# Performance work log

Measured on AMD Instinct MI355X. Metric: run time of the kernel, lower is better.

Reference implementation:

```python
import jax, jax.numpy as jnp
from jax import lax
import numpy as np

B, N, NP, NS = 32, 4096, 512, 16
C = 256            # seed_feat_dim
RADIUS = 0.3
EPS = 1e-5         # BatchNorm eps
HID = 128


def setup_inputs() -> dict:
    key = jax.random.key(0)
    ks = jax.random.split(key, 8)
    xyz = jax.random.normal(ks[0], (B, N, 3), jnp.float32)
    features = jax.random.normal(ks[1], (B, C, N), jnp.float32)
    seed_xyz = jax.random.normal(ks[2], (B, N, 3), jnp.float32)
    c_in = C + 3  # use_xyz=True -> mlp[0] += 3
    def conv_w(k, cin, cout):
        return jax.random.normal(k, (cout, cin), jnp.float32) * (1.0 / np.sqrt(cin))
    w1 = conv_w(ks[3], c_in, HID)
    w2 = conv_w(ks[4], HID, HID)
    w3 = conv_w(ks[5], HID, HID)
    ones = jnp.ones((HID,), jnp.float32)
    zeros = jnp.zeros((HID,), jnp.float32)
    return dict(xyz=xyz, features=features, seed_xyz=seed_xyz,
                w1=w1, g1=ones, be1=zeros,
                w2=w2, g2=ones, be2=zeros,
                w3=w3, g3=ones, be3=zeros)


def furthest_point_sample(pts, npoint):
    # pts: (B, N, 3) -> (B, npoint) int32
    Bb, Nn, _ = pts.shape
    first = jnp.zeros((Bb,), jnp.int32)
    dists0 = jnp.full((Bb, Nn), 1e10, pts.dtype)
    def step(carry, _):
        dists, last = carry
        lp = jnp.take_along_axis(pts, last[:, None, None], axis=1)  # (B,1,3)
        d = jnp.sum((pts - lp) ** 2, axis=-1)                        # (B,N)
        dists = jnp.minimum(dists, d)
        nxt = jnp.argmax(dists, axis=-1).astype(jnp.int32)
        return (dists, nxt), nxt
    _, rest = lax.scan(step, (dists0, first), None, length=npoint - 1)
    return jnp.concatenate([first[None, :], rest], axis=0).T  # (B, npoint)


def ball_query(new_xyz, xyz, radius, nsample):
    # new_xyz: (B,NP,3), xyz: (B,N,3) -> (B,NP,nsample) int32
    d2 = jnp.sum((new_xyz[:, :, None, :] - xyz[:, None, :, :]) ** 2, axis=-1)  # (B,NP,N)
    Nn = xyz.shape[1]
    # first `nsample` indices (in index order) inside radius, like the CUDA kernel
    score = jnp.where(d2 < radius * radius, jnp.arange(Nn, dtype=jnp.int32)[None, None, :], Nn)
    neg_vals, _ = lax.top_k(-score, nsample)   # largest of -score = smallest indices
    idx = -neg_vals                            # (B,NP,nsample)
    valid = idx < Nn
    idx = jnp.where(valid, idx, idx[:, :, 0:1])  # pad with first hit (query point itself)
    return idx


def _conv_bn_relu(x, w, g, be):
    # x: (B,Cin,NP,NS); 1x1 Conv2d (no bias, bn=True) + BatchNorm2d (training stats) + ReLU
    y = jnp.einsum('oc,bcps->bops', w, x)
    m = y.mean(axis=(0, 2, 3))
    v = y.var(axis=(0, 2, 3))
    y = (y - m[None, :, None, None]) * (g / jnp.sqrt(v + EPS))[None, :, None, None] + be[None, :, None, None]
    return jax.nn.relu(y)


def reference(xyz, features, seed_xyz, w1, g1, be1, w2, g2, be2, w3, g3, be3):
    # sampling == 'seed_fps'
    sample_inds = furthest_point_sample(seed_xyz, NP)                 # (B,NP)
    new_xyz = jnp.take_along_axis(xyz, sample_inds[:, :, None], axis=1)  # (B,NP,3)
    idx = ball_query(new_xyz, xyz, RADIUS, NS)                        # (B,NP,NS)
    grouped_xyz = jax.vmap(lambda p, i: p[i])(xyz, idx)               # (B,NP,NS,3)
    grouped_xyz = (grouped_xyz - new_xyz[:, :, None, :]) / RADIUS     # normalize_xyz=True
    grouped_feat = jax.vmap(lambda f, i: f[:, i])(features, idx)      # (B,C,NP,NS)
    x = jnp.concatenate([grouped_xyz.transpose(0, 3, 1, 2), grouped_feat], axis=1)  # (B,3+C,NP,NS)
    x = _conv_bn_relu(x, w1, g1, be1)
    x = _conv_bn_relu(x, w2, g2, be2)
    x = _conv_bn_relu(x, w3, g3, be3)
    new_features = jnp.max(x, axis=-1)                                # (B,128,NP)
    return new_xyz, new_features, sample_inds
```

## Files before the change

### kernel.cpp

```cpp
#include <hip/hip_runtime.h>
#include <cstdint>
#include <cstddef>

#define B   32
#define N   4096
#define NP  512
#define NS  16
#define C   256
#define CIN 259
#define HID 128
#define SB  (NP*NS)
#define S   (B*SB)
#define EPSF 1e-5f

#define FPS_BLOCKS 32
#define TR_BLOCKS  (B*256)
#define PREP_BLOCKS 64

typedef __attribute__((ext_vector_type(8))) short short8;
typedef __attribute__((ext_vector_type(4))) float floatx4;

__device__ __forceinline__ float bf2f(unsigned short u) {
    return __uint_as_float(((unsigned)u) << 16);
}
__device__ __forceinline__ unsigned short f2bf(float f) {
    unsigned u = __float_as_uint(f);
    return (unsigned short)((u + 0x7FFFu + ((u >> 16) & 1u)) >> 16);
}

__device__ __forceinline__ int wave_max_i32(int x) {
    int y;
    y = __builtin_amdgcn_update_dpp(0, x, 0x111, 0xf, 0xf, true); x = (y > x) ? y : x;
    y = __builtin_amdgcn_update_dpp(0, x, 0x112, 0xf, 0xf, true); x = (y > x) ? y : x;
    y = __builtin_amdgcn_update_dpp(0, x, 0x114, 0xf, 0xf, true); x = (y > x) ? y : x;
    y = __builtin_amdgcn_update_dpp(0, x, 0x118, 0xf, 0xf, true); x = (y > x) ? y : x;
    y = __builtin_amdgcn_update_dpp(0, x, 0x142, 0xa, 0xf, true); x = (y > x) ? y : x;
    y = __builtin_amdgcn_update_dpp(0, x, 0x143, 0xc, 0xf, true); x = (y > x) ? y : x;
    return __builtin_amdgcn_readlane(x, 63);
}
__device__ __forceinline__ unsigned wave_max_u32(unsigned x) {
    unsigned y;
    y = (unsigned)__builtin_amdgcn_update_dpp(0, (int)x, 0x111, 0xf, 0xf, true); x = (y > x) ? y : x;
    y = (unsigned)__builtin_amdgcn_update_dpp(0, (int)x, 0x112, 0xf, 0xf, true); x = (y > x) ? y : x;
    y = (unsigned)__builtin_amdgcn_update_dpp(0, (int)x, 0x114, 0xf, 0xf, true); x = (y > x) ? y : x;
    y = (unsigned)__builtin_amdgcn_update_dpp(0, (int)x, 0x118, 0xf, 0xf, true); x = (y > x) ? y : x;
    y = (unsigned)__builtin_amdgcn_update_dpp(0, (int)x, 0x142, 0xa, 0xf, true); x = (y > x) ? y : x;
    y = (unsigned)__builtin_amdgcn_update_dpp(0, (int)x, 0x143, 0xc, 0xf, true); x = (y > x) ? y : x;
    return (unsigned)__builtin_amdgcn_readlane((int)x, 63);
}

__device__ __forceinline__ unsigned long long umax64(unsigned long long a, unsigned long long b) {
    return (b > a) ? b : a;
}

__global__ __launch_bounds__(512) void fused_front_kernel(
        const float* __restrict__ seed, const float* __restrict__ xyz,
        const float* __restrict__ feat, const float* __restrict__ w1,
        const float* __restrict__ w2, const float* __restrict__ w3,
        unsigned short* __restrict__ featT, unsigned short* __restrict__ w1fb,
        unsigned short* __restrict__ w2b, unsigned short* __restrict__ w3b,
        float* __restrict__ stats, int* __restrict__ inds,
        float* __restrict__ out_newxyz, float* __restrict__ out_inds_f) {
    __shared__ float smem[3 * N];
    __shared__ __align__(16) unsigned long long skey[2][8];
    __shared__ __align__(16) float4 scoord[2][8];
    __shared__ int lhist[NP];
    int bid = blockIdx.x;
    int t = threadIdx.x;

    if (bid >= FPS_BLOCKS) {
        int hb = bid - FPS_BLOCKS;
        if (hb < TR_BLOCKS) {
            float* ls = smem;
            int b2 = hb >> 8, rem = hb & 255;
            int ct = rem >> 5, jt = rem & 31;
            int c0 = ct * 32, j0 = jt * 128;
            const float* src = feat + (size_t)b2 * C * N;
            #pragma unroll
            for (int i = 0; i < 8; i++) {
                int lin = t + 512 * i;
                int jj = lin & 127, cc = lin >> 7;
                ls[cc * 129 + jj] = src[(size_t)(c0 + cc) * N + j0 + jj];
            }
            __syncthreads();
            int c8 = t & 3, jj = t >> 2;
            unsigned pk[4];
            #pragma unroll
            for (int q = 0; q < 4; q++) {
                float f0 = ls[(c8 * 8 + 2 * q) * 129 + jj];
                float f1 = ls[(c8 * 8 + 2 * q + 1) * 129 + jj];
                pk[q] = (unsigned)f2bf(f0) | ((unsigned)f2bf(f1) << 16);
            }
            *(uint4*)&featT[((size_t)b2 * N + j0 + jj) * 256 + c0 + c8 * 8] =
                make_uint4(pk[0], pk[1], pk[2], pk[3]);
        } else {
            int i0 = (hb - TR_BLOCKS) * 512 + t;
            if (i0 < 256 * HID) { int o = i0 >> 8, k = i0 & 255; w1fb[i0] = f2bf(w1[o * CIN + 3 + k]); }
            if (i0 < HID * HID) { w2b[i0] = f2bf(w2[i0]); w3b[i0] = f2bf(w3[i0]); }
            if (i0 < 3 * 512) stats[i0] = 0.f;
        }
        return;
    }

    int b = bid;
    const float* sp = seed + (size_t)b * N * 3;
    float px[8], py[8], pz[8], dloc[8];
    #pragma unroll
    for (int u = 0; u < 8; u++) {
        int i = t + 512 * u;
        px[u] = sp[i * 3 + 0]; py[u] = sp[i * 3 + 1]; pz[u] = sp[i * 3 + 2];
        dloc[u] = 1e10f;
    }
    if (t == 0) lhist[0] = 0;
    float lx = sp[0], ly = sp[1], lz = sp[2];
    int lane = t & 63, w = t >> 6;
    for (int k = 1; k < NP; k++) {
        float bv = -1.f; int bi = 0;
        float bx = 0.f, by = 0.f, bz = 0.f;
        #pragma unroll
        for (int u = 0; u < 8; u++) {
            int i = t + 512 * u;
            float dx = __fsub_rn(px[u], lx);
            float dy = __fsub_rn(py[u], ly);
            float dz = __fsub_rn(pz[u], lz);
            float d  = __fadd_rn(__fadd_rn(__fmul_rn(dx, dx), __fmul_rn(dy, dy)), __fmul_rn(dz, dz));
            float dm = fminf(dloc[u], d);
            dloc[u] = dm;
            bool bt = dm > bv;
            bv = bt ? dm : bv;
            bi = bt ? i : bi;
            bx = bt ? px[u] : bx;
            by = bt ? py[u] : by;
            bz = bt ? pz[u] : bz;
        }
        int wm = wave_max_i32(__float_as_int(bv));
        unsigned cand = (__float_as_int(bv) == wm) ? ~(unsigned)bi : 0u;
        unsigned winv = wave_max_u32(cand);
        int wbi = (int)(~winv);
        int par = k & 1;
        if (lane == (wbi & 63)) {
            skey[par][w] = (((unsigned long long)(unsigned)wm) << 12) | (unsigned)(4095 - wbi);
            scoord[par][w] = make_float4(bx, by, bz, 0.f);
        }
        __syncthreads();
        const ulonglong2* kp = (const ulonglong2*)&skey[par][0];
        ulonglong2 q0 = kp[0], q1 = kp[1], q2 = kp[2], q3 = kp[3];
        unsigned long long a = umax64(q0.x, q0.y);
        unsigned long long c2 = umax64(q1.x, q1.y);
        unsigned long long e = umax64(q2.x, q2.y);
        unsigned long long g = umax64(q3.x, q3.y);
        unsigned long long h = umax64(umax64(a, c2), umax64(e, g));
        int gi = 4095 - (int)(h & 0xFFFull);
        int ws = (gi & 511) >> 6;
        float4 wc = scoord[par][ws];
        lx = wc.x; ly = wc.y; lz = wc.z;
        if (t == 0) lhist[k] = gi;
    }
    __syncthreads();
    {
        int p = t;
        int j = lhist[p];
        const float* xb = xyz + ((size_t)b * N + j) * 3;
        float* ob = out_newxyz + ((size_t)b * NP + p) * 3;
        ob[0] = xb[0]; ob[1] = xb[1]; ob[2] = xb[2];
        out_inds_f[b * NP + p] = (float)j;
    }
}

__global__ __launch_bounds__(256) void ballquery_kernel(const float* __restrict__ xyz,
        const float* __restrict__ newxyz, int* __restrict__ idx) {
    __shared__ float sx[N], sy[N], sz[N];
    int blk = blockIdx.x;
    int b   = blk >> 5;
    int q00 = (blk & 31) * 16;
    int t = threadIdx.x, lane = t & 63, w = t >> 6;
    const float* xb = xyz + (size_t)b * N * 3;
    for (int i = t; i < N; i += 256) { sx[i] = xb[i * 3]; sy[i] = xb[i * 3 + 1]; sz[i] = xb[i * 3 + 2]; }
    __syncthreads();
    for (int qi = 0; qi < 4; qi++) {
        int q = q00 + w * 4 + qi;
        const float* nq = newxyz + ((size_t)(b * NP + q)) * 3;
        float qx = nq[0], qy = nq[1], qz = nq[2];
        int* out = idx + ((size_t)(b * NP + q)) * NS;
        int cnt = 0, first = -1;
        for (int it = 0; it < 64; it++) {
            int j = it * 64 + lane;
            float dx = __fsub_rn(sx[j], qx);
            float dy = __fsub_rn(sy[j], qy);
            float dz = __fsub_rn(sz[j], qz);
            float d2 = __fadd_rn(__fadd_rn(__fmul_rn(dx, dx), __fmul_rn(dy, dy)), __fmul_rn(dz, dz));
            bool inb = d2 < 0.09f;
            unsigned long long m = __ballot(inb);
            if (m) {
                if (first < 0) first = it * 64 + __builtin_ctzll(m);
                if (inb) {
                    int r = cnt + __popcll(m & ((1ull << lane) - 1ull));
                    if (r < NS) out[r] = j;
                }
                cnt += __popcll(m);
                if (cnt >= NS) break;
            }
        }
        if (cnt < NS && lane >= cnt && lane < NS) out[lane] = first;
    }
}

__global__ __launch_bounds__(256) void gemm1_mfma(
        const unsigned short* __restrict__ w1fb, const float* __restrict__ w1raw,
        const unsigned short* __restrict__ featT, const float* __restrict__ newxyz,
        const float* __restrict__ xyz, const int* __restrict__ idx,
        unsigned short* __restrict__ y1) {
    __shared__ unsigned short Xs[128][136];
    __shared__ float xn0[128], xn1[128], xn2[128];
    __shared__ int jl[128];
    int t = threadIdx.x;
    int s0 = blockIdx.x * 128;
    int b = s0 >> 13;
    if (t < 128) {
        int pn = (s0 & (SB - 1)) + t;
        int p = pn >> 4, n = pn & 15;
        int j = idx[((size_t)(b * NP + p)) * NS + n];
        jl[t] = j;
        const float* xb = xyz + ((size_t)(b * N + j)) * 3;
        const float* nq = newxyz + ((size_t)(b * NP + p)) * 3;
        xn0[t] = (xb[0] - nq[0]) / 0.3f;
        xn1[t] = (xb[1] - nq[1]) / 0.3f;
        xn2[t] = (xb[2] - nq[2]) / 0.3f;
    }
    __syncthreads();
    int lane = t & 63, w = t >> 6;
    int row16 = lane & 15, quad = lane >> 4;
    floatx4 acc[2][8];
    #pragma unroll
    for (int mt = 0; mt < 2; mt++)
        #pragma unroll
        for (int nt = 0; nt < 8; nt++)
            acc[mt][nt] = (floatx4){0.f, 0.f, 0.f, 0.f};
    int ss = t >> 1, hh = (t & 1) * 64;
    const unsigned short* grow = featT + ((size_t)b * N + jl[ss]) * 256 + hh;
    for (int slab = 0; slab < 2; slab++) {
        int k0 = slab * 128;
        {
            const uint4* src = (const uint4*)(grow + k0);
            #pragma unroll
            for (int i = 0; i < 8; i++)
                *(uint4*)&Xs[ss][hh + i * 8] = src[i];
        }
        __syncthreads();
        #pragma unroll
        for (int kk = 0; kk < 128; kk += 32) {
            short8 a0 = *(const short8*)&w1fb[(size_t)(w * 32 + row16) * 256 + k0 + kk + quad * 8];
            short8 a1 = *(const short8*)&w1fb[(size_t)(w * 32 + 16 + row16) * 256 + k0 + kk + quad * 8];
            #pragma unroll
            for (int nt = 0; nt < 8; nt++) {
                short8 bf = *(const short8*)&Xs[nt * 16 + row16][kk + quad * 8];
                acc[0][nt] = __builtin_amdgcn_mfma_f32_16x16x32_bf16(a0, bf, acc[0][nt], 0, 0, 0);
                acc[1][nt] = __builtin_amdgcn_mfma_f32_16x16x32_bf16(a1, bf, acc[1][nt], 0, 0, 0);
            }
        }
        __syncthreads();
    }
    float wa[8], wbv[8], wc[8];
    #pragma unroll
    for (int mt = 0; mt < 2; mt++)
        #pragma unroll
        for (int r = 0; r < 4; r++) {
            int o = w * 32 + mt * 16 + quad * 4 + r;
            const float* wr = w1raw + (size_t)o * CIN;
            wa[mt * 4 + r] = wr[0]; wbv[mt * 4 + r] = wr[1]; wc[mt * 4 + r] = wr[2];
        }
    float x0l[8], x1l[8], x2l[8];
    #pragma unroll
    for (int nt = 0; nt < 8; nt++) {
        int s = nt * 16 + row16;
        x0l[nt] = xn0[s]; x1l[nt] = xn1[s]; x2l[nt] = xn2[s];
    }
    #pragma unroll
    for (int mt = 0; mt < 2; mt++)
        #pragma unroll
        for (int nt = 0; nt < 8; nt++) {
            int s = nt * 16 + row16;
            int ob = w * 32 + mt * 16 + quad * 4;
            floatx4 a = acc[mt][nt];
            float v0 = a[0] + wa[mt*4+0]*x0l[nt] + wbv[mt*4+0]*x1l[nt] + wc[mt*4+0]*x2l[nt];
            float v1 = a[1] + wa[mt*4+1]*x0l[nt] + wbv[mt*4+1]*x1l[nt] + wc[mt*4+1]*x2l[nt];
            float v2 = a[2] + wa[mt*4+2]*x0l[nt] + wbv[mt*4+2]*x1l[nt] + wc[mt*4+2]*x2l[nt];
            float v3 = a[3] + wa[mt*4+3]*x0l[nt] + wbv[mt*4+3]*x1l[nt] + wc[mt*4+3]*x2l[nt];
            unsigned p0 = (unsigned)f2bf(v0) | ((unsigned)f2bf(v1) << 16);
            unsigned p1 = (unsigned)f2bf(v2) | ((unsigned)f2bf(v3) << 16);
            *(uint2*)&Xs[s][ob] = make_uint2(p0, p1);
        }
    __syncthreads();
    int c = t & 15, sr = t >> 4;
    #pragma unroll
    for (int i = 0; i < 8; i++) {
        int s = sr + 16 * i;
        uint4 v = *(const uint4*)&Xs[s][c * 8];
        *(uint4*)&y1[(size_t)(s0 + s) * 128 + c * 8] = v;
    }
}

__global__ __launch_bounds__(256) void gemm_bn_mfma(
        const unsigned short* __restrict__ wb16, const unsigned short* __restrict__ yprev,
        const float* __restrict__ statsPrev, unsigned short* __restrict__ yout) {
    __shared__ unsigned short Xs[128][136];
    __shared__ float ssc[128], ssh[128];
    int t = threadIdx.x;
    int s0 = blockIdx.x * 128;
    if (t < 128) { ssc[t] = statsPrev[256 + t]; ssh[t] = statsPrev[384 + t]; }
    __syncthreads();
    int ss = t >> 1, hh = (t & 1) * 64;
    {
        const uint4* src = (const uint4*)&yprev[(size_t)(s0 + ss) * 128 + hh];
        #pragma unroll
        for (int i = 0; i < 8; i++) {
            uint4 raw = src[i];
            int kb = hh + i * 8;
            float4 c0 = *(float4*)&ssc[kb];
            float4 c1 = *(float4*)&ssc[kb + 4];
            float4 h0 = *(float4*)&ssh[kb];
            float4 h1 = *(float4*)&ssh[kb + 4];
            float f0 = fmaxf(0.f, fmaf(bf2f((unsigned short)(raw.x & 0xFFFF)), c0.x, h0.x));
            float f1 = fmaxf(0.f, fmaf(bf2f((unsigned short)(raw.x >> 16)),    c0.y, h0.y));
            float f2 = fmaxf(0.f, fmaf(bf2f((unsigned short)(raw.y & 0xFFFF)), c0.z, h0.z));
            float f3 = fmaxf(0.f, fmaf(bf2f((unsigned short)(raw.y >> 16)),    c0.w, h0.w));
            float f4 = fmaxf(0.f, fmaf(bf2f((unsigned short)(raw.z & 0xFFFF)), c1.x, h1.x));
            float f5 = fmaxf(0.f, fmaf(bf2f((unsigned short)(raw.z >> 16)),    c1.y, h1.y));
            float f6 = fmaxf(0.f, fmaf(bf2f((unsigned short)(raw.w & 0xFFFF)), c1.z, h1.z));
            float f7 = fmaxf(0.f, fmaf(bf2f((unsigned short)(raw.w >> 16)),    c1.w, h1.w));
            unsigned o0 = (unsigned)f2bf(f0) | ((unsigned)f2bf(f1) << 16);
            unsigned o1 = (unsigned)f2bf(f2) | ((unsigned)f2bf(f3) << 16);
            unsigned o2 = (unsigned)f2bf(f4) | ((unsigned)f2bf(f5) << 16);
            unsigned o3 = (unsigned)f2bf(f6) | ((unsigned)f2bf(f7) << 16);
            *(uint4*)&Xs[ss][kb] = make_uint4(o0, o1, o2, o3);
        }
    }
    __syncthreads();
    int lane = t & 63, w = t >> 6;
    int row16 = lane & 15, quad = lane >> 4;
    floatx4 acc[2][8];
    #pragma unroll
    for (int mt = 0; mt < 2; mt++)
        #pragma unroll
        for (int nt = 0; nt < 8; nt++)
            acc[mt][nt] = (floatx4){0.f, 0.f, 0.f, 0.f};
    #pragma unroll
    for (int kk = 0; kk < 128; kk += 32) {
        short8 a0 = *(const short8*)&wb16[(size_t)(w * 32 + row16) * 128 + kk + quad * 8];
        short8 a1 = *(const short8*)&wb16[(size_t)(w * 32 + 16 + row16) * 128 + kk + quad * 8];
        #pragma unroll
        for (int nt = 0; nt < 8; nt++) {
            short8 bf = *(const short8*)&Xs[nt * 16 + row16][kk + quad * 8];
            acc[0][nt] = __builtin_amdgcn_mfma_f32_16x16x32_bf16(a0, bf, acc[0][nt], 0, 0, 0);
            acc[1][nt] = __builtin_amdgcn_mfma_f32_16x16x32_bf16(a1, bf, acc[1][nt], 0, 0, 0);
        }
    }
    __syncthreads();
    #pragma unroll
    for (int mt = 0; mt < 2; mt++)
        #pragma unroll
        for (int nt = 0; nt < 8; nt++) {
            int s = nt * 16 + row16;
            int ob = w * 32 + mt * 16 + quad * 4;
            floatx4 a = acc[mt][nt];
            unsigned p0 = (unsigned)f2bf(a[0]) | ((unsigned)f2bf(a[1]) << 16);
            unsigned p1 = (unsigned)f2bf(a[2]) | ((unsigned)f2bf(a[3]) << 16);
            *(uint2*)&Xs[s][ob] = make_uint2(p0, p1);
        }
    __syncthreads();
    int c = t & 15, sr = t >> 4;
    #pragma unroll
    for (int i = 0; i < 8; i++) {
        int s = sr + 16 * i;
        uint4 v = *(const uint4*)&Xs[s][c * 8];
        *(uint4*)&yout[(size_t)(s0 + s) * 128 + c * 8] = v;
    }
}

__global__ __launch_bounds__(256) void stats_kernel(const unsigned short* __restrict__ y,
                                                    float* __restrict__ st) {
    __shared__ float ls[128], lq[128];
    int t = threadIdx.x;
    if (t < 128) { ls[t] = 0.f; lq[t] = 0.f; }
    __syncthreads();
    int c = t & 15, r0 = t >> 4;
    float s8[8] = {}, q8[8] = {};
    size_t base0 = (size_t)blockIdx.x * 512;
    for (int i = 0; i < 32; i++) {
        size_t s = base0 + r0 + (size_t)i * 16;
        uint4 v = *(const uint4*)&y[s * 128 + c * 8];
        unsigned ww[4] = {v.x, v.y, v.z, v.w};
        #pragma unroll
        for (int j = 0; j < 4; j++) {
            float f0 = bf2f((unsigned short)(ww[j] & 0xFFFF));
            float f1 = bf2f((unsigned short)(ww[j] >> 16));
            s8[2*j]   += f0; q8[2*j]   = fmaf(f0, f0, q8[2*j]);
            s8[2*j+1] += f1; q8[2*j+1] = fmaf(f1, f1, q8[2*j+1]);
        }
    }
    #pragma unroll
    for (int j = 0; j < 8; j++) {
        atomicAdd(&ls[c * 8 + j], s8[j]);
        atomicAdd(&lq[c * 8 + j], q8[j]);
    }
    __syncthreads();
    if (t < 128) { atomicAdd(&st[t], ls[t]); atomicAdd(&st[128 + t], lq[t]); }
}

__global__ void bnparam_kernel(float* __restrict__ stats, const float* __restrict__ g,
                               const float* __restrict__ be) {
    int o = threadIdx.x;
    float mean = stats[o] * (1.f / (float)S);
    float var  = stats[128 + o] * (1.f / (float)S) - mean * mean;
    float sc = g[o] / sqrtf(var + EPSF);
    stats[256 + o] = sc;
    stats[384 + o] = be[o] - mean * sc;
}

__global__ __launch_bounds__(256) void maxpool_kernel(const unsigned short* __restrict__ y3,
        const float* __restrict__ st, float* __restrict__ out1) {
    int g = blockIdx.x * 256 + threadIdx.x;
    int p = g & 511;
    int oc = (g >> 9) & 15;
    int b = g >> 13;
    float sc[8], sh[8];
    #pragma unroll
    for (int j = 0; j < 8; j++) { sc[j] = st[256 + oc * 8 + j]; sh[j] = st[384 + oc * 8 + j]; }
    float m[8];
    #pragma unroll
    for (int j = 0; j < 8; j++) m[j] = 0.f;
    size_t base = ((size_t)(b * NP + p) * NS) * 128 + oc * 8;
    #pragma unroll
    for (int n = 0; n < 16; n++) {
        uint4 v = *(const uint4*)&y3[base + (size_t)n * 128];
        unsigned ww[4] = {v.x, v.y, v.z, v.w};
        #pragma unroll
        for (int j = 0; j < 4; j++) {
            m[2*j]   = fmaxf(m[2*j],   fmaf(bf2f((unsigned short)(ww[j] & 0xFFFF)), sc[2*j],   sh[2*j]));
            m[2*j+1] = fmaxf(m[2*j+1], fmaf(bf2f((unsigned short)(ww[j] >> 16)),    sc[2*j+1], sh[2*j+1]));
        }
    }
    #pragma unroll
    for (int j = 0; j < 8; j++)
        out1[((size_t)b * HID + oc * 8 + j) * NP + p] = m[j];
}

extern "C" void kernel_launch(void* const* d_in, const int* in_sizes, int n_in,
                              void* d_out, int out_size, void* d_ws, size_t ws_size,
                              hipStream_t stream) {
    const float* xyz  = (const float*)d_in[0];
    const float* feat = (const float*)d_in[1];
    const float* seed = (const float*)d_in[2];
    const float* w1 = (const float*)d_in[3];
    const float* g1 = (const float*)d_in[4];
    const float* be1 = (const float*)d_in[5];
    const float* w2 = (const float*)d_in[6];
    const float* g2 = (const float*)d_in[7];
    const float* be2 = (const float*)d_in[8];
    const float* w3 = (const float*)d_in[9];
    const float* g3 = (const float*)d_in[10];
    const float* be3 = (const float*)d_in[11];

    float* out_newxyz = (float*)d_out;
    float* out_feat   = out_newxyz + B * NP * 3;
    float* out_inds   = out_feat + B * HID * NP;

    float* stats = (float*)d_ws;
    int*   inds  = (int*)(stats + 3 * 512);
    int*   idx   = inds + B * NP;
    unsigned short* w1fb  = (unsigned short*)(idx + (size_t)B * NP * NS);
    unsigned short* w2b   = w1fb + 256 * HID;
    unsigned short* w3b   = w2b + HID * HID;
    unsigned short* featT = w3b + HID * HID;
    unsigned short* y1    = featT + (size_t)B * N * 256;
    unsigned short* y2    = featT;
    unsigned short* y3    = y1;

    size_t need = (size_t)(3 * 512) * 4 + (size_t)B * NP * 4 + (size_t)B * NP * NS * 4
                + (size_t)(256 * HID + 2 * HID * HID) * 2
                + 2ull * (size_t)B * N * 256 * 2;
    if (ws_size < need) return;

    fused_front_kernel<<<FPS_BLOCKS + TR_BLOCKS + PREP_BLOCKS, 512, 0, stream>>>(
        seed, xyz, feat, w1, w2, w3, featT, w1fb, w2b, w3b, stats,
        inds, out_newxyz, out_inds);
    ballquery_kernel<<<B * 32, 256, 0, stream>>>(xyz, out_newxyz, idx);
    gemm1_mfma<<<S / 128, 256, 0, stream>>>(w1fb, w1, featT, out_newxyz, xyz, idx, y1);
    stats_kernel<<<512, 256, 0, stream>>>(y1, stats);
    bnparam_kernel<<<1, HID, 0, stream>>>(stats, g1, be1);
    gemm_bn_mfma<<<S / 128, 256, 0, stream>>>(w2b, y1, stats, y2);
    stats_kernel<<<512, 256, 0, stream>>>(y2, stats + 512);
    bnparam_kernel<<<1, HID, 0, stream>>>(stats + 512, g2, be2);
    gemm_bn_mfma<<<S / 128, 256, 0, stream>>>(w3b, y2, stats + 512, y3);
    stats_kernel<<<512, 256, 0, stream>>>(y3, stats + 1024);
    bnparam_kernel<<<1, HID, 0, stream>>>(stats + 1024, g3, be3);
    maxpool_kernel<<<(B * 16 * NP) / 256, 256, 0, stream>>>(y3, stats + 1024, out_feat);
}
```

Measured before the change: 855.0 us.

## Fuse BN statistics into GEMM epilogues and max-pool into the third GEMM

```diff
diff --git a/kernel.cpp b/kernel.cpp
--- a/kernel.cpp
+++ b/kernel.cpp
@@ -51,6 +51,24 @@
 
 __device__ __forceinline__ unsigned long long umax64(unsigned long long a, unsigned long long b) {
     return (b > a) ? b : a;
+}
+
+__device__ __forceinline__ float row16_sum(float x) {
+    float y;
+    y = __int_as_float(__builtin_amdgcn_update_dpp(0, __float_as_int(x), 0x111, 0xf, 0xf, true)); x += y;
+    y = __int_as_float(__builtin_amdgcn_update_dpp(0, __float_as_int(x), 0x112, 0xf, 0xf, true)); x += y;
+    y = __int_as_float(__builtin_amdgcn_update_dpp(0, __float_as_int(x), 0x114, 0xf, 0xf, true)); x += y;
+    y = __int_as_float(__builtin_amdgcn_update_dpp(0, __float_as_int(x), 0x118, 0xf, 0xf, true)); x += y;
+    return x;
+}
+__device__ __forceinline__ float row16_max(float x) {
+    int xi = __float_as_int(x);
+    float y;
+    y = __int_as_float(__builtin_amdgcn_update_dpp(xi, xi, 0x111, 0xf, 0xf, false)); x = fmaxf(x, y); xi = __float_as_int(x);
+    y = __int_as_float(__builtin_amdgcn_update_dpp(xi, xi, 0x112, 0xf, 0xf, false)); x = fmaxf(x, y); xi = __float_as_int(x);
+    y = __int_as_float(__builtin_amdgcn_update_dpp(xi, xi, 0x114, 0xf, 0xf, false)); x = fmaxf(x, y); xi = __float_as_int(x);
+    y = __int_as_float(__builtin_amdgcn_update_dpp(xi, xi, 0x118, 0xf, 0xf, false)); x = fmaxf(x, y);
+    return x;
 }
 
 __global__ __launch_bounds__(512) void fused_front_kernel(
@@ -209,7 +227,7 @@
         const unsigned short* __restrict__ w1fb, const float* __restrict__ w1raw,
         const unsigned short* __restrict__ featT, const float* __restrict__ newxyz,
         const float* __restrict__ xyz, const int* __restrict__ idx,
-        unsigned short* __restrict__ y1) {
+        unsigned short* __restrict__ y1, float* __restrict__ statsOut) {
     __shared__ unsigned short Xs[128][136];
     __shared__ float xn0[128], xn1[128], xn2[128];
     __shared__ int jl[128];
@@ -275,6 +293,7 @@
         int s = nt * 16 + row16;
         x0l[nt] = xn0[s]; x1l[nt] = xn1[s]; x2l[nt] = xn2[s];
     }
+    float s8[2][4] = {}, q8[2][4] = {};
     #pragma unroll
     for (int mt = 0; mt < 2; mt++)
         #pragma unroll
@@ -286,9 +305,25 @@
             float v1 = a[1] + wa[mt*4+1]*x0l[nt] + wbv[mt*4+1]*x1l[nt] + wc[mt*4+1]*x2l[nt];
             float v2 = a[2] + wa[mt*4+2]*x0l[nt] + wbv[mt*4+2]*x1l[nt] + wc[mt*4+2]*x2l[nt];
             float v3 = a[3] + wa[mt*4+3]*x0l[nt] + wbv[mt*4+3]*x1l[nt] + wc[mt*4+3]*x2l[nt];
+            s8[mt][0] += v0; q8[mt][0] = fmaf(v0, v0, q8[mt][0]);
+            s8[mt][1] += v1; q8[mt][1] = fmaf(v1, v1, q8[mt][1]);
+            s8[mt][2] += v2; q8[mt][2] = fmaf(v2, v2, q8[mt][2]);
+            s8[mt][3] += v3; q8[mt][3] = fmaf(v3, v3, q8[mt][3]);
             unsigned p0 = (unsigned)f2bf(v0) | ((unsigned)f2bf(v1) << 16);
             unsigned p1 = (unsigned)f2bf(v2) | ((unsigned)f2bf(v3) << 16);
             *(uint2*)&Xs[s][ob] = make_uint2(p0, p1);
+        }
+    #pragma unroll
+    for (int mt = 0; mt < 2; mt++)
+        #pragma unroll
+        for (int r = 0; r < 4; r++) {
+            float sv = row16_sum(s8[mt][r]);
+            float qv = row16_sum(q8[mt][r]);
+            if ((lane & 15) == 15) {
+                int o = w * 32 + mt * 16 + quad * 4 + r;
+                atomicAdd(&statsOut[o], sv);
+                atomicAdd(&statsOut[128 + o], qv);
+            }
         }
     __syncthreads();
     int c = t & 15, sr = t >> 4;
@@ -302,12 +337,20 @@
 
 __global__ __launch_bounds__(256) void gemm_bn_mfma(
         const unsigned short* __restrict__ wb16, const unsigned short* __restrict__ yprev,
-        const float* __restrict__ statsPrev, unsigned short* __restrict__ yout) {
+        const float* __restrict__ statsPrev, const float* __restrict__ gPrev,
+        const float* __restrict__ bePrev, float* __restrict__ statsOut,
+        unsigned short* __restrict__ yout) {
     __shared__ unsigned short Xs[128][136];
     __shared__ float ssc[128], ssh[128];
     int t = threadIdx.x;
     int s0 = blockIdx.x * 128;
-    if (t < 128) { ssc[t] = statsPrev[256 + t]; ssh[t] = statsPrev[384 + t]; }
+    if (t < 128) {
+        float mean = statsPrev[t] * (1.f / (float)S);
+        float var  = statsPrev[128 + t] * (1.f / (float)S) - mean * mean;
+        float sc = gPrev[t] / sqrtf(var + EPSF);
+        ssc[t] = sc;
+        ssh[t] = bePrev[t] - mean * sc;
+    }
     __syncthreads();
     int ss = t >> 1, hh = (t & 1) * 64;
     {
@@ -356,6 +399,7 @@
         }
     }
     __syncthreads();
+    float s8[2][4] = {}, q8[2][4] = {};
     #pragma unroll
     for (int mt = 0; mt < 2; mt++)
         #pragma unroll
@@ -363,9 +407,25 @@
             int s = nt * 16 + row16;
             int ob = w * 32 + mt * 16 + quad * 4;
             floatx4 a = acc[mt][nt];
+            s8[mt][0] += a[0]; q8[mt][0] = fmaf(a[0], a[0], q8[mt][0]);
+            s8[mt][1] += a[1]; q8[mt][1] = fmaf(a[1], a[1], q8[mt][1]);
+            s8[mt][2] += a[2]; q8[mt][2] = fmaf(a[2], a[2], q8[mt][2]);
+            s8[mt][3] += a[3]; q8[mt][3] = fmaf(a[3], a[3], q8[mt][3]);
             unsigned p0 = (unsigned)f2bf(a[0]) | ((unsigned)f2bf(a[1]) << 16);
             unsigned p1 = (unsigned)f2bf(a[2]) | ((unsigned)f2bf(a[3]) << 16);
             *(uint2*)&Xs[s][ob] = make_uint2(p0, p1);
+        }
+    #pragma unroll
+    for (int mt = 0; mt < 2; mt++)
+        #pragma unroll
+        for (int r = 0; r < 4; r++) {
+            float sv = row16_sum(s8[mt][r]);
+            float qv = row16_sum(q8[mt][r]);
+            if ((lane & 15) == 15) {
+                int o = w * 32 + mt * 16 + quad * 4 + r;
+                atomicAdd(&statsOut[o], sv);
+                atomicAdd(&statsOut[128 + o], qv);
+            }
         }
     __syncthreads();
     int c = t & 15, sr = t >> 4;
@@ -377,72 +437,124 @@
     }
 }
 
-__global__ __launch_bounds__(256) void stats_kernel(const unsigned short* __restrict__ y,
-                                                    float* __restrict__ st) {
-    __shared__ float ls[128], lq[128];
+__global__ __launch_bounds__(256) void gemm3_pool_mfma(
+        const unsigned short* __restrict__ wb16, const unsigned short* __restrict__ yprev,
+        const float* __restrict__ statsPrev, const float* __restrict__ gPrev,
+        const float* __restrict__ bePrev, float* __restrict__ statsOut,
+        float* __restrict__ out_feat) {
+    __shared__ unsigned short Xs[128][136];
+    __shared__ float ssc[128], ssh[128];
+    __shared__ float pool[8][133];
     int t = threadIdx.x;
-    if (t < 128) { ls[t] = 0.f; lq[t] = 0.f; }
-    __syncthreads();
-    int c = t & 15, r0 = t >> 4;
-    float s8[8] = {}, q8[8] = {};
-    size_t base0 = (size_t)blockIdx.x * 512;
-    for (int i = 0; i < 32; i++) {
-        size_t s = base0 + r0 + (size_t)i * 16;
-        uint4 v = *(const uint4*)&y[s * 128 + c * 8];
-        unsigned ww[4] = {v.x, v.y, v.z, v.w};
-        #pragma unroll
-        for (int j = 0; j < 4; j++) {
-            float f0 = bf2f((unsigned short)(ww[j] & 0xFFFF));
-            float f1 = bf2f((unsigned short)(ww[j] >> 16));
-            s8[2*j]   += f0; q8[2*j]   = fmaf(f0, f0, q8[2*j]);
-            s8[2*j+1] += f1; q8[2*j+1] = fmaf(f1, f1, q8[2*j+1]);
-        }
-    }
-    #pragma unroll
-    for (int j = 0; j < 8; j++) {
-        atomicAdd(&ls[c * 8 + j], s8[j]);
-        atomicAdd(&lq[c * 8 + j], q8[j]);
-    }
-    __syncthreads();
-    if (t < 128) { atomicAdd(&st[t], ls[t]); atomicAdd(&st[128 + t], lq[t]); }
-}
-
-__global__ void bnparam_kernel(float* __restrict__ stats, const float* __restrict__ g,
-                               const float* __restrict__ be) {
-    int o = threadIdx.x;
-    float mean = stats[o] * (1.f / (float)S);
-    float var  = stats[128 + o] * (1.f / (float)S) - mean * mean;
+    int s0 = blockIdx.x * 128;
+    if (t < 128) {
+        float mean = statsPrev[t] * (1.f / (float)S);
+        float var  = statsPrev[128 + t] * (1.f / (float)S) - mean * mean;
+        float sc = gPrev[t] / sqrtf(var + EPSF);
+        ssc[t] = sc;
+        ssh[t] = bePrev[t] - mean * sc;
+    }
+    __syncthreads();
+    int ss = t >> 1, hh = (t & 1) * 64;
+    {
+        const uint4* src = (const uint4*)&yprev[(size_t)(s0 + ss) * 128 + hh];
+        #pragma unroll
+        for (int i = 0; i < 8; i++) {
+            uint4 raw = src[i];
+            int kb = hh + i * 8;
+            float4 c0 = *(float4*)&ssc[kb];
+            float4 c1 = *(float4*)&ssc[kb + 4];
+            float4 h0 = *(float4*)&ssh[kb];
+            float4 h1 = *(float4*)&ssh[kb + 4];
+            float f0 = fmaxf(0.f, fmaf(bf2f((unsigned short)(raw.x & 0xFFFF)), c0.x, h0.x));
+            float f1 = fmaxf(0.f, fmaf(bf2f((unsigned short)(raw.x >> 16)),    c0.y, h0.y));
+            float f2 = fmaxf(0.f, fmaf(bf2f((unsigned short)(raw.y & 0xFFFF)), c0.z, h0.z));
+            float f3 = fmaxf(0.f, fmaf(bf2f((unsigned short)(raw.y >> 16)),    c0.w, h0.w));
+            float f4 = fmaxf(0.f, fmaf(bf2f((unsigned short)(raw.z & 0xFFFF)), c1.x, h1.x));
+            float f5 = fmaxf(0.f, fmaf(bf2f((unsigned short)(raw.z >> 16)),    c1.y, h1.y));
+            float f6 = fmaxf(0.f, fmaf(bf2f((unsigned short)(raw.w & 0xFFFF)), c1.z, h1.z));
+            float f7 = fmaxf(0.f, fmaf(bf2f((unsigned short)(raw.w >> 16)),    c1.w, h1.w));
+            unsigned o0 = (unsigned)f2bf(f0) | ((unsigned)f2bf(f1) << 16);
+            unsigned o1 = (unsigned)f2bf(f2) | ((unsigned)f2bf(f3) << 16);
+            unsigned o2 = (unsigned)f2bf(f4) | ((unsigned)f2bf(f5) << 16);
+            unsigned o3 = (unsigned)f2bf(f6) | ((unsigned)f2bf(f7) << 16);
+            *(uint4*)&Xs[ss][kb] = make_uint4(o0, o1, o2, o3);
+        }
+    }
+    __syncthreads();
+    int lane = t & 63, w = t >> 6;
+    int row16 = lane & 15, quad = lane >> 4;
+    floatx4 acc[2][8];
+    #pragma unroll
+    for (int mt = 0; mt < 2; mt++)
+        #pragma unroll
+        for (int nt = 0; nt < 8; nt++)
+            acc[mt][nt] = (floatx4){0.f, 0.f, 0.f, 0.f};
+    #pragma unroll
+    for (int kk = 0; kk < 128; kk += 32) {
+        short8 a0 = *(const short8*)&wb16[(size_t)(w * 32 + row16) * 128 + kk + quad * 8];
+        short8 a1 = *(const short8*)&wb16[(size_t)(w * 32 + 16 + row16) * 128 + kk + quad * 8];
+        #pragma unroll
+        for (int nt = 0; nt < 8; nt++) {
+            short8 bf = *(const short8*)&Xs[nt * 16 + row16][kk + quad * 8];
+            acc[0][nt] = __builtin_amdgcn_mfma_f32_16x16x32_bf16(a0, bf, acc[0][nt], 0, 0, 0);
+            acc[1][nt] = __builtin_amdgcn_mfma_f32_16x16x32_bf16(a1, bf, acc[1][nt], 0, 0, 0);
+        }
+    }
+    float s8[2][4] = {}, q8[2][4] = {};
+    #pragma unroll
+    for (int mt = 0; mt < 2; mt++)
+        #pragma unroll
+        for (int nt = 0; nt < 8; nt++) {
+            floatx4 a = acc[mt][nt];
+            #pragma unroll
+            for (int r = 0; r < 4; r++) {
+                float v = a[r];
+                s8[mt][r] += v;
+                q8[mt][r] = fmaf(v, v, q8[mt][r]);
+                float mx = row16_max(v);
+                if ((lane & 15) == 15)
+                    pool[nt][w * 32 + mt * 16 + quad * 4 + r] = mx;
+            }
+        }
+    #pragma unroll
+    for (int mt = 0; mt < 2; mt++)
+        #pragma unroll
+        for (int r = 0; r < 4; r++) {
+            float sv = row16_sum(s8[mt][r]);
+            float qv = row16_sum(q8[mt][r]);
+            if ((lane & 15) == 15) {
+                int o = w * 32 + mt * 16 + quad * 4 + r;
+                atomicAdd(&statsOut[o], sv);
+                atomicAdd(&statsOut[128 + o], qv);
+            }
+        }
+    __syncthreads();
+    {
+        int b = s0 >> 13;
+        int pcol0 = (s0 & (SB - 1)) >> 4;
+        int o = t >> 1, half = (t & 1) * 4;
+        float4 v = make_float4(pool[half + 0][o], pool[half + 1][o],
+                               pool[half + 2][o], pool[half + 3][o]);
+        *(float4*)&out_feat[((size_t)b * HID + o) * NP + pcol0 + half] = v;
+    }
+}
+
+__global__ __launch_bounds__(256) void finalize_kernel(float* __restrict__ out_feat,
+        const float* __restrict__ st3, const float* __restrict__ g,
+        const float* __restrict__ be) {
+    int i = (blockIdx.x * 256 + threadIdx.x) * 4;
+    int o = (i >> 9) & 127;
+    float mean = st3[o] * (1.f / (float)S);
+    float var  = st3[128 + o] * (1.f / (float)S) - mean * mean;
     float sc = g[o] / sqrtf(var + EPSF);
-    stats[256 + o] = sc;
-    stats[384 + o] = be[o] - mean * sc;
-}
-
-__global__ __launch_bounds__(256) void maxpool_kernel(const unsigned short* __restrict__ y3,
-        const float* __restrict__ st, float* __restrict__ out1) {
-    int g = blockIdx.x * 256 + threadIdx.x;
-    int p = g & 511;
-    int oc = (g >> 9) & 15;
-    int b = g >> 13;
-    float sc[8], sh[8];
-    #pragma unroll
-    for (int j = 0; j < 8; j++) { sc[j] = st[256 + oc * 8 + j]; sh[j] = st[384 + oc * 8 + j]; }
-    float m[8];
-    #pragma unroll
-    for (int j = 0; j < 8; j++) m[j] = 0.f;
-    size_t base = ((size_t)(b * NP + p) * NS) * 128 + oc * 8;
-    #pragma unroll
-    for (int n = 0; n < 16; n++) {
-        uint4 v = *(const uint4*)&y3[base + (size_t)n * 128];
-        unsigned ww[4] = {v.x, v.y, v.z, v.w};
-        #pragma unroll
-        for (int j = 0; j < 4; j++) {
-            m[2*j]   = fmaxf(m[2*j],   fmaf(bf2f((unsigned short)(ww[j] & 0xFFFF)), sc[2*j],   sh[2*j]));
-            m[2*j+1] = fmaxf(m[2*j+1], fmaf(bf2f((unsigned short)(ww[j] >> 16)),    sc[2*j+1], sh[2*j+1]));
-        }
-    }
-    #pragma unroll
-    for (int j = 0; j < 8; j++)
-        out1[((size_t)b * HID + oc * 8 + j) * NP + p] = m[j];
+    float sh = be[o] - mean * sc;
+    float4 v = *(float4*)&out_feat[i];
+    v.x = fmaxf(0.f, fmaf(v.x, sc, sh));
+    v.y = fmaxf(0.f, fmaf(v.y, sc, sh));
+    v.z = fmaxf(0.f, fmaf(v.z, sc, sh));
+    v.w = fmaxf(0.f, fmaf(v.w, sc, sh));
+    *(float4*)&out_feat[i] = v;
 }
 
 extern "C" void kernel_launch(void* const* d_in, const int* in_sizes, int n_in,
@@ -474,7 +586,6 @@
     unsigned short* featT = w3b + HID * HID;
     unsigned short* y1    = featT + (size_t)B * N * 256;
     unsigned short* y2    = featT;
-    unsigned short* y3    = y1;
 
     size_t need = (size_t)(3 * 512) * 4 + (size_t)B * NP * 4 + (size_t)B * NP * NS * 4
                 + (size_t)(256 * HID + 2 * HID * HID) * 2
@@ -485,14 +596,8 @@
         seed, xyz, feat, w1, w2, w3, featT, w1fb, w2b, w3b, stats,
         inds, out_newxyz, out_inds);
     ballquery_kernel<<<B * 32, 256, 0, stream>>>(xyz, out_newxyz, idx);
-    gemm1_mfma<<<S / 128, 256, 0, stream>>>(w1fb, w1, featT, out_newxyz, xyz, idx, y1);
-    stats_kernel<<<512, 256, 0, stream>>>(y1, stats);
-    bnparam_kernel<<<1, HID, 0, stream>>>(stats, g1, be1);
-    gemm_bn_mfma<<<S / 128, 256, 0, stream>>>(w2b, y1, stats, y2);
-    stats_kernel<<<512, 256, 0, stream>>>(y2, stats + 512);
-    bnparam_kernel<<<1, HID, 0, stream>>>(stats + 512, g2, be2);
-    gemm_bn_mfma<<<S / 128, 256, 0, stream>>>(w3b, y2, stats + 512, y3);
-    stats_kernel<<<512, 256, 0, stream>>>(y3, stats + 1024);
-    bnparam_kernel<<<1, HID, 0, stream>>>(stats + 1024, g3, be3);
-    maxpool_kernel<<<(B * 16 * NP) / 256, 256, 0, stream>>>(y3, stats + 1024, out_feat);
-}
+    gemm1_mfma<<<S / 128, 256, 0, stream>>>(w1fb, w1, featT, out_newxyz, xyz, idx, y1, stats);
+    gemm_bn_mfma<<<S / 128, 256, 0, stream>>>(w2b, y1, stats, g1, be1, stats + 256, y2);
+    gemm3_pool_mfma<<<S / 128, 256, 0, stream>>>(w3b, y2, stats + 256, g2, be2, stats + 512, out_feat);
+    finalize_kernel<<<(B * HID * NP) / 1024, 256, 0, stream>>>(out_feat, stats + 512, g3, be3);
+}
```

Result: slower. 1.238 ms (+44.8%).
